# Performance work log

Measured on AMD Instinct MI355X. Metric: run time of the kernel, lower is better.

The kernel has to match this reference:

```python
import jax, jax.numpy as jnp
import numpy as np

B, S, E = 8, 4096, 512
QKV, H = 512, 8
D = QKV // H  # head_dim = 64
EPS = 1e-6


def setup_inputs() -> dict:
    key = jax.random.key(0)
    ks = jax.random.split(key, 9)
    sc_in = 1.0 / np.sqrt(E)
    sc_qkv = 1.0 / np.sqrt(QKV)
    # Linear weights stored as [in, out] so y = x @ W + b (equivalent to torch x @ W_t.T + b)
    return {
        "x": jax.random.normal(ks[0], (B, S, E), dtype=jnp.float32),
        "Wq": jax.random.uniform(ks[1], (E, QKV), jnp.float32, -sc_in, sc_in),
        "bq": jax.random.uniform(ks[2], (QKV,), jnp.float32, -sc_in, sc_in),
        "Wk": jax.random.uniform(ks[3], (E, QKV), jnp.float32, -sc_in, sc_in),
        "bk": jax.random.uniform(ks[4], (QKV,), jnp.float32, -sc_in, sc_in),
        "Wv": jax.random.uniform(ks[5], (E, QKV), jnp.float32, -sc_in, sc_in),
        "bv": jax.random.uniform(ks[6], (QKV,), jnp.float32, -sc_in, sc_in),
        "Wo": jax.random.uniform(ks[7], (QKV, E), jnp.float32, -sc_qkv, sc_qkv),
        "bo": jax.random.uniform(ks[8], (E,), jnp.float32, -sc_qkv, sc_qkv),
    }


def feature_map(t):
    # elu(x) + 1 (always positive features)
    return jax.nn.elu(t) + 1.0


def reference(x, Wq, bq, Wk, bk, Wv, bv, Wo, bo):
    bs, seqlen, _ = x.shape
    q = (x @ Wq + bq).reshape(bs, seqlen, H, D)
    k = (x @ Wk + bk).reshape(bs, seqlen, H, D)
    v = (x @ Wv + bv).reshape(bs, seqlen, H, D)
    q = feature_map(q)
    k = feature_map(k)
    # kv: [n, h, m, d] -- per-head outer-product accumulation over sequence
    kv = jnp.einsum('nshd,nshm->nhmd', k, v)
    # normalizer z: [n, l, h]
    z = 1.0 / (jnp.einsum('nlhd,nhd->nlh', q, k.sum(axis=1)) + EPS)
    out = jnp.einsum('nlhd,nhmd,nlh->nlhm', q, kv, z)
    out = out.reshape(bs, seqlen, QKV)
    return out @ Wo + bo
```

## Files before the change

kernel.cpp:

```cpp
#include <hip/hip_runtime.h>
#include <hip/hip_bf16.h>


typedef __bf16 bf16x8 __attribute__((ext_vector_type(8)));
typedef float  f32x4  __attribute__((ext_vector_type(4)));

__device__ __forceinline__ float b2f(unsigned short u) {
    unsigned int x = ((unsigned int)u) << 16;
    return __builtin_bit_cast(float, x);
}
__device__ __forceinline__ unsigned short f2b(float f) {
    unsigned int u = __builtin_bit_cast(unsigned int, f);
    unsigned int r = (u + 0x7FFFu + ((u >> 16) & 1u)) >> 16;
    return (unsigned short)r;
}
__device__ __forceinline__ void load_lds16(const unsigned short* g, unsigned short* l) {
    __builtin_amdgcn_global_load_lds(
        (const __attribute__((address_space(1))) void*)g,
        (__attribute__((address_space(3))) void*)l, 16, 0, 0);
}

__global__ void prep_kernel(const float* __restrict__ x,
                            const float* __restrict__ w0, const float* __restrict__ w1,
                            const float* __restrict__ w2, const float* __restrict__ w3,
                            unsigned short* __restrict__ xb, unsigned short* __restrict__ wt,
                            float* __restrict__ ksg, float* __restrict__ kvg) {
    __shared__ float tile[64][65];
    int t = threadIdx.x;
    if (blockIdx.x >= 256) {
        int i = (blockIdx.x - 256) * 256 + t;
        float4 v = ((const float4*)x)[i];
        ushort4 o;
        o.x = f2b(v.x); o.y = f2b(v.y); o.z = f2b(v.z); o.w = f2b(v.w);
        ((ushort4*)xb)[i] = o;
        return;
    }
    int idx = blockIdx.x;
    if (idx < 16) ksg[idx * 256 + t] = 0.f;
    ((float4*)kvg)[idx * 256 + t] = (float4){0.f, 0.f, 0.f, 0.f};
    int bz = idx >> 6, by = (idx >> 3) & 7, bx = idx & 7;
    const float* src = (bz == 0) ? w0 : (bz == 1) ? w1 : (bz == 2) ? w2 : w3;
    unsigned short* dst = wt + (size_t)bz * 512 * 512;
    int rb = by * 64, cb = bx * 64;
    #pragma unroll
    for (int i = 0; i < 16; i++) {
        int c = t + i * 256; int r = c >> 6, cc = c & 63;
        tile[r][cc] = src[(rb + r) * 512 + cb + cc];
    }
    __syncthreads();
    #pragma unroll
    for (int i = 0; i < 16; i++) {
        int c = t + i * 256; int r = c >> 6, cc = c & 63;
        dst[(cb + r) * 512 + rb + cc] = f2b(tile[cc][r]);
    }
}

__global__ __launch_bounds__(256, 4) void gemm_qkv_kernel(
        const unsigned short* __restrict__ xb, const unsigned short* __restrict__ wt,
        const float* __restrict__ bq, const float* __restrict__ bk, const float* __restrict__ bv,
        unsigned short* __restrict__ qb, unsigned short* __restrict__ kT,
        unsigned short* __restrict__ vT, float* __restrict__ ksg) {
    int g = blockIdx.x;
    int xcd = g & 7, slot = g >> 3;
    int mtile = xcd * 32 + slot / 12;
    int tn = slot % 12;
    int tensor = tn >> 2, ntile = tn & 3;
    const unsigned short* Bt = wt + (size_t)tensor * 512 * 512;
    const float* bias = tensor == 0 ? bq : tensor == 1 ? bk : bv;
    bool act = tensor < 2;

    __shared__ __align__(16) unsigned short sA[128 * 64];
    __shared__ __align__(16) unsigned short sB[128 * 64];
    const int tid  = threadIdx.x;
    const int wave = tid >> 6, lane = tid & 63;
    const int wm = wave >> 1, wn = wave & 1;
    const int quad = lane >> 4, l16 = lane & 15;
    const int mbase = mtile * 128, nbase = ntile * 128;
    const int rsub = lane >> 3;
    const int coff = (((lane & 7) ^ rsub) << 3);

    f32x4 acc[4][4];
    #pragma unroll
    for (int i = 0; i < 4; i++)
        #pragma unroll
        for (int j = 0; j < 4; j++) acc[i][j] = (f32x4){0.f, 0.f, 0.f, 0.f};

    for (int kb = 0; kb < 512; kb += 64) {
        #pragma unroll
        for (int t = 0; t < 4; t++) {
            int r0 = t * 32 + wave * 8;
            load_lds16(&xb[(size_t)(mbase + r0 + rsub) * 512 + kb + coff], &sA[r0 * 64]);
            load_lds16(&Bt[(size_t)(nbase + r0 + rsub) * 512 + kb + coff], &sB[r0 * 64]);
        }
        __syncthreads();
        #pragma unroll
        for (int ko = 0; ko < 64; ko += 32) {
            bf16x8 af[4], bfr[4];
            int pg = ((quad + (ko >> 3)) ^ (l16 & 7)) << 3;
            #pragma unroll
            for (int f = 0; f < 4; f++)
                af[f] = *(const bf16x8*)&sA[(wm * 64 + f * 16 + l16) * 64 + pg];
            #pragma unroll
            for (int f = 0; f < 4; f++)
                bfr[f] = *(const bf16x8*)&sB[(wn * 64 + f * 16 + l16) * 64 + pg];
            #pragma unroll
            for (int i = 0; i < 4; i++)
                #pragma unroll
                for (int j = 0; j < 4; j++)
                    acc[i][j] = __builtin_amdgcn_mfma_f32_16x16x32_bf16(af[i], bfr[j], acc[i][j], 0, 0, 0);
        }
        __syncthreads();
    }
    if (tensor == 0) {
        #pragma unroll
        for (int i = 0; i < 4; i++)
            #pragma unroll
            for (int j = 0; j < 4; j++) {
                int gcol = nbase + wn * 64 + j * 16 + l16;
                float bv = bias[gcol];
                #pragma unroll
                for (int r = 0; r < 4; r++) {
                    int grow = mbase + wm * 64 + i * 16 + quad * 4 + r;
                    float v = acc[i][j][r] + bv;
                    v = v > 0.f ? v + 1.f : __expf(v);
                    qb[(size_t)grow * 512 + gcol] = f2b(v);
                }
            }
    } else {
        unsigned short* T = (tensor == 1) ? kT : vT;
        float csum[4] = {0.f, 0.f, 0.f, 0.f};
        #pragma unroll
        for (int i = 0; i < 4; i++)
            #pragma unroll
            for (int j = 0; j < 4; j++) {
                int gcol = nbase + wn * 64 + j * 16 + l16;
                int h = gcol >> 6, d = gcol & 63;
                float bv = bias[gcol];
                int grow0 = mbase + wm * 64 + i * 16 + quad * 4;
                int b = grow0 >> 12, s0 = grow0 & 4095;
                ushort4 o;
                #pragma unroll
                for (int r = 0; r < 4; r++) {
                    float v = acc[i][j][r] + bv;
                    if (act) { v = v > 0.f ? v + 1.f : __expf(v); csum[j] += v; }
                    ((unsigned short*)&o)[r] = f2b(v);
                }
                *(ushort4*)&T[(((size_t)b * 8 + h) * 64 + d) * 4096 + s0] = o;
            }
        if (act) {
            int b = mbase >> 12;
            #pragma unroll
            for (int j = 0; j < 4; j++) {
                float s = csum[j];
                s += __shfl_xor(s, 16, 64);
                s += __shfl_xor(s, 32, 64);
                if (quad == 0) {
                    int gcol = nbase + wn * 64 + j * 16 + l16;
                    atomicAdd(&ksg[b * 512 + gcol], s);
                }
            }
        }
    }
}

__global__ __launch_bounds__(256, 2) void kv_kernel(
        const unsigned short* __restrict__ kT, const unsigned short* __restrict__ vT,
        float* __restrict__ kvg) {
    int bh = blockIdx.x >> 3, sc = blockIdx.x & 7;
    const int tid = threadIdx.x;
    const int wave = tid >> 6, lane = tid & 63;
    const int wm = wave >> 1, wn = wave & 1;
    const int quad = lane >> 4, l16 = lane & 15;
    const int rsub = lane >> 3;
    const int coff = (((lane & 7) ^ rsub) << 3);
    __shared__ __align__(16) unsigned short sV[2][64 * 64];
    __shared__ __align__(16) unsigned short sK[2][64 * 64];

    f32x4 acc[2][2];
    #pragma unroll
    for (int i = 0; i < 2; i++)
        #pragma unroll
        for (int j = 0; j < 2; j++) acc[i][j] = (f32x4){0.f, 0.f, 0.f, 0.f};
    size_t base = (size_t)bh * 64 * 4096 + sc * 512;

    auto stage = [&](int kb, int buf) {
        int s0 = kb * 64;
        #pragma unroll
        for (int t = 0; t < 2; t++) {
            int r0 = t * 32 + wave * 8;
            load_lds16(&vT[base + (size_t)(r0 + rsub) * 4096 + s0 + coff], &sV[buf][r0 * 64]);
            load_lds16(&kT[base + (size_t)(r0 + rsub) * 4096 + s0 + coff], &sK[buf][r0 * 64]);
        }
    };

    stage(0, 0);
    for (int kb = 0; kb < 8; kb++) {
        int buf = kb & 1;
        if (kb < 7) {
            stage(kb + 1, buf ^ 1);
            asm volatile("s_waitcnt vmcnt(4)" ::: "memory");
        } else {
            asm volatile("s_waitcnt vmcnt(0)" ::: "memory");
        }
        __builtin_amdgcn_sched_barrier(0);
        __builtin_amdgcn_s_barrier();
        #pragma unroll
        for (int ko = 0; ko < 64; ko += 32) {
            bf16x8 af[2], bfr[2];
            int pg = ((quad + (ko >> 3)) ^ (l16 & 7)) << 3;
            #pragma unroll
            for (int f = 0; f < 2; f++)
                af[f] = *(const bf16x8*)&sV[buf][(wm * 32 + f * 16 + l16) * 64 + pg];
            #pragma unroll
            for (int f = 0; f < 2; f++)
                bfr[f] = *(const bf16x8*)&sK[buf][(wn * 32 + f * 16 + l16) * 64 + pg];
            #pragma unroll
            for (int i = 0; i < 2; i++)
                #pragma unroll
                for (int j = 0; j < 2; j++)
                    acc[i][j] = __builtin_amdgcn_mfma_f32_16x16x32_bf16(af[i], bfr[j], acc[i][j], 0, 0, 0);
        }
        __builtin_amdgcn_s_barrier();
        __builtin_amdgcn_sched_barrier(0);
    }
    float* out = kvg + (size_t)bh * 4096;
    #pragma unroll
    for (int i = 0; i < 2; i++)
        #pragma unroll
        for (int j = 0; j < 2; j++)
            #pragma unroll
            for (int r = 0; r < 4; r++) {
                int m = wm * 32 + i * 16 + quad * 4 + r;
                int d = wn * 32 + j * 16 + l16;
                atomicAdd(&out[m * 64 + d], acc[i][j][r]);
            }
}

__global__ __launch_bounds__(256, 2) void fused_out_kernel(
        const unsigned short* __restrict__ qb,
        const float* __restrict__ kvg, const float* __restrict__ ksg,
        const unsigned short* __restrict__ wto, const float* __restrict__ bo,
        float* __restrict__ out) {
    int g = blockIdx.x;
    int xcd = g & 7, slot = g >> 3;
    int mtile = xcd * 32 + (slot >> 1);
    int np = slot & 1;

    __shared__ __align__(16) unsigned short sQ[128 * 64];
    __shared__ __align__(16) unsigned short sWo[2][128 * 64];
    __shared__ __align__(16) unsigned short sKV[64 * 64];
    __shared__ __align__(16) unsigned short sO1[128 * 64];
    __shared__ float sKsum[512];
    __shared__ float sZ[128];
    const int tid  = threadIdx.x;
    const int wave = tid >> 6, lane = tid & 63;
    const int wm = wave >> 1, wn = wave & 1;
    const int quad = lane >> 4, l16 = lane & 15;
    const int mbase = mtile * 128, nbase = np * 256;
    const int b = mtile >> 5;
    const int rsub = lane >> 3;
    const int coff = (((lane & 7) ^ rsub) << 3);

    sKsum[tid]       = ksg[b * 512 + tid];
    sKsum[tid + 256] = ksg[b * 512 + 256 + tid];

    f32x4 accm[2][4][4];
    #pragma unroll
    for (int n = 0; n < 2; n++)
        #pragma unroll
        for (int i = 0; i < 4; i++)
            #pragma unroll
            for (int j = 0; j < 4; j++) accm[n][i][j] = (f32x4){0.f, 0.f, 0.f, 0.f};

    for (int h = 0; h < 8; h++) {
        #pragma unroll
        for (int t = 0; t < 4; t++) {
            int r0 = t * 32 + wave * 8;
            load_lds16(&qb[(size_t)(mbase + r0 + rsub) * 512 + h * 64 + coff], &sQ[r0 * 64]);
            load_lds16(&wto[(size_t)(nbase + r0 + rsub) * 512 + h * 64 + coff], &sWo[0][r0 * 64]);
            load_lds16(&wto[(size_t)(nbase + 128 + r0 + rsub) * 512 + h * 64 + coff], &sWo[1][r0 * 64]);
        }
        #pragma unroll
        for (int oi = 0; oi < 2; oi++) {
            int idx = tid + oi * 256;
            int row = idx >> 3, G = idx & 7;
            const float4* src = (const float4*)&kvg[((size_t)(b * 8 + h)) * 4096 + row * 64 + G * 8];
            float4 a = src[0], c = src[1];
            unsigned int p0 = (unsigned int)f2b(a.x) | ((unsigned int)f2b(a.y) << 16);
            unsigned int p1 = (unsigned int)f2b(a.z) | ((unsigned int)f2b(a.w) << 16);
            unsigned int p2 = (unsigned int)f2b(c.x) | ((unsigned int)f2b(c.y) << 16);
            unsigned int p3 = (unsigned int)f2b(c.z) | ((unsigned int)f2b(c.w) << 16);
            *(uint4*)&sKV[row * 64 + ((G ^ (row & 7)) << 3)] = (uint4){p0, p1, p2, p3};
        }
        __syncthreads();
        {
            int row = tid >> 1, half = tid & 1;
            const float* ksh = &sKsum[h * 64];
            float dsum = 0.f;
            #pragma unroll
            for (int g2 = 0; g2 < 4; g2++) {
                int G = half * 4 + g2;
                uint4 w = *(const uint4*)&sQ[row * 64 + ((G ^ (row & 7)) << 3)];
                const unsigned int* qp = (const unsigned int*)&w;
                #pragma unroll
                for (int u = 0; u < 4; u++) {
                    int c = G * 8 + u * 2;
                    dsum += __builtin_bit_cast(float, qp[u] << 16)        * ksh[c];
                    dsum += __builtin_bit_cast(float, qp[u] & 0xFFFF0000u) * ksh[c + 1];
                }
            }
            dsum += __shfl_xor(dsum, 1, 64);
            if (!half) sZ[row] = 1.f / (dsum + 1e-6f);
        }
        __syncthreads();
        f32x4 acco[4][2];
        #pragma unroll
        for (int f = 0; f < 4; f++)
            #pragma unroll
            for (int j = 0; j < 2; j++) acco[f][j] = (f32x4){0.f, 0.f, 0.f, 0.f};
        #pragma unroll
        for (int ko = 0; ko < 64; ko += 32) {
            bf16x8 af[4], bfr[2];
            int pg = ((quad + (ko >> 3)) ^ (l16 & 7)) << 3;
            #pragma unroll
            for (int f = 0; f < 4; f++)
                af[f] = *(const bf16x8*)&sQ[(wm * 64 + f * 16 + l16) * 64 + pg];
            #pragma unroll
            for (int j = 0; j < 2; j++)
                bfr[j] = *(const bf16x8*)&sKV[(wn * 32 + j * 16 + l16) * 64 + pg];
            #pragma unroll
            for (int f = 0; f < 4; f++)
                #pragma unroll
                for (int j = 0; j < 2; j++)
                    acco[f][j] = __builtin_amdgcn_mfma_f32_16x16x32_bf16(af[f], bfr[j], acco[f][j], 0, 0, 0);
        }
        #pragma unroll
        for (int f = 0; f < 4; f++)
            #pragma unroll
            for (int j = 0; j < 2; j++)
                #pragma unroll
                for (int r = 0; r < 4; r++) {
                    int row = wm * 64 + f * 16 + quad * 4 + r;
                    int col = wn * 32 + j * 16 + l16;
                    float v = acco[f][j][r] * sZ[row];
                    int grp = col >> 3;
                    sO1[row * 64 + ((grp ^ (row & 7)) << 3) + (col & 7)] = f2b(v);
                }
        __syncthreads();
        #pragma unroll
        for (int ko = 0; ko < 64; ko += 32) {
            bf16x8 af[4], bfr0[4], bfr1[4];
            int pg = ((quad + (ko >> 3)) ^ (l16 & 7)) << 3;
            #pragma unroll
            for (int f = 0; f < 4; f++)
                af[f] = *(const bf16x8*)&sO1[(wm * 64 + f * 16 + l16) * 64 + pg];
            #pragma unroll
            for (int f = 0; f < 4; f++) {
                bfr0[f] = *(const bf16x8*)&sWo[0][(wn * 64 + f * 16 + l16) * 64 + pg];
                bfr1[f] = *(const bf16x8*)&sWo[1][(wn * 64 + f * 16 + l16) * 64 + pg];
            }
            #pragma unroll
            for (int i = 0; i < 4; i++)
                #pragma unroll
                for (int j = 0; j < 4; j++) {
                    accm[0][i][j] = __builtin_amdgcn_mfma_f32_16x16x32_bf16(af[i], bfr0[j], accm[0][i][j], 0, 0, 0);
                    accm[1][i][j] = __builtin_amdgcn_mfma_f32_16x16x32_bf16(af[i], bfr1[j], accm[1][i][j], 0, 0, 0);
                }
        }
        __syncthreads();
    }
    #pragma unroll
    for (int n = 0; n < 2; n++)
        #pragma unroll
        for (int i = 0; i < 4; i++)
            #pragma unroll
            for (int j = 0; j < 4; j++) {
                int gcol = nbase + n * 128 + wn * 64 + j * 16 + l16;
                float bv = bo[gcol];
                #pragma unroll
                for (int r = 0; r < 4; r++) {
                    int grow = mbase + wm * 64 + i * 16 + quad * 4 + r;
                    out[(size_t)grow * 512 + gcol] = accm[n][i][j][r] + bv;
                }
            }
}

extern "C" void kernel_launch(void* const* d_in, const int* in_sizes, int n_in,
                              void* d_out, int out_size, void* d_ws, size_t ws_size,
                              hipStream_t stream) {
    const float* x  = (const float*)d_in[0];
    const float* Wq = (const float*)d_in[1];
    const float* bq = (const float*)d_in[2];
    const float* Wk = (const float*)d_in[3];
    const float* bk = (const float*)d_in[4];
    const float* Wv = (const float*)d_in[5];
    const float* bv = (const float*)d_in[6];
    const float* Wo = (const float*)d_in[7];
    const float* bo = (const float*)d_in[8];
    float* out = (float*)d_out;

    char* wsb = (char*)d_ws;
    char* ob  = (char*)d_out;
    unsigned short* vT  = (unsigned short*)ob;
    unsigned short* xb  = (unsigned short*)(ob + 33554432ull);
    unsigned short* qb  = (unsigned short*)wsb;
    unsigned short* kT  = (unsigned short*)(wsb + 33554432ull);
    unsigned short* wt  = (unsigned short*)(wsb + 67108864ull);
    float*          kvg = (float*)(wsb + 69206016ull);
    float*          ksg = (float*)(wsb + 70254592ull);

    prep_kernel<<<16640, 256, 0, stream>>>(x, Wq, Wk, Wv, Wo, xb, wt, ksg, kvg);
    gemm_qkv_kernel<<<3072, 256, 0, stream>>>(xb, wt, bq, bk, bv, qb, kT, vT, ksg);
    kv_kernel<<<512, 256, 0, stream>>>(kT, vT, kvg);
    fused_out_kernel<<<512, 256, 0, stream>>>(qb, kvg, ksg,
            wt + 3ull * 512 * 512, bo, out);
}
```

Baseline: 249.2 us.

## Fuse K/V projection with per-tile KV outer-product accumulation in LDS

Splits the QKV projection into a Q-only GEMM and a K/V kernel that computes K and V tiles in sequence for the same row tile. The K/V tiles are kept in swizzled LDS, and their per-head outer product is accumulated into kv with atomics. This removes the global write and re-read of the transposed K and V tensors and drops the separate kv kernel. In exchange it adds many more float atomics into kv (one set per 128-row tile) and uses more LDS, which lowers occupancy to 2 blocks per CU.

Result: no change. 252.7 us (+1.4%).

```diff
diff --git a/kernel.cpp b/kernel.cpp
--- a/kernel.cpp
+++ b/kernel.cpp
@@ -5,10 +5,6 @@
 typedef __bf16 bf16x8 __attribute__((ext_vector_type(8)));
 typedef float  f32x4  __attribute__((ext_vector_type(4)));
 
-__device__ __forceinline__ float b2f(unsigned short u) {
-    unsigned int x = ((unsigned int)u) << 16;
-    return __builtin_bit_cast(float, x);
-}
 __device__ __forceinline__ unsigned short f2b(float f) {
     unsigned int u = __builtin_bit_cast(unsigned int, f);
     unsigned int r = (u + 0x7FFFu + ((u >> 16) & 1u)) >> 16;
@@ -55,19 +51,159 @@
     }
 }
 
-__global__ __launch_bounds__(256, 4) void gemm_qkv_kernel(
+__global__ __launch_bounds__(256, 2) void gemm_kv_kernel(
         const unsigned short* __restrict__ xb, const unsigned short* __restrict__ wt,
-        const float* __restrict__ bq, const float* __restrict__ bk, const float* __restrict__ bv,
-        unsigned short* __restrict__ qb, unsigned short* __restrict__ kT,
-        unsigned short* __restrict__ vT, float* __restrict__ ksg) {
+        const float* __restrict__ bk, const float* __restrict__ bv,
+        float* __restrict__ ksg, float* __restrict__ kvg) {
     int g = blockIdx.x;
     int xcd = g & 7, slot = g >> 3;
-    int mtile = xcd * 32 + slot / 12;
-    int tn = slot % 12;
-    int tensor = tn >> 2, ntile = tn & 3;
-    const unsigned short* Bt = wt + (size_t)tensor * 512 * 512;
-    const float* bias = tensor == 0 ? bq : tensor == 1 ? bk : bv;
-    bool act = tensor < 2;
+    int mtile = xcd * 32 + (slot >> 2);
+    int ntile = slot & 3;
+
+    __shared__ __align__(16) unsigned short sStage[16384];
+    __shared__ __align__(16) unsigned short sKT[16384];
+    unsigned short* sA = sStage;
+    unsigned short* sB = sStage + 8192;
+
+    const int tid  = threadIdx.x;
+    const int wave = tid >> 6, lane = tid & 63;
+    const int wm = wave >> 1, wn = wave & 1;
+    const int quad = lane >> 4, l16 = lane & 15;
+    const int mbase = mtile * 128, nbase = ntile * 128;
+    const int rsub = lane >> 3;
+    const int coff = (((lane & 7) ^ rsub) << 3);
+    const int b = mtile >> 5;
+
+    f32x4 acc[4][4];
+
+    auto run_pass = [&](const unsigned short* Bt) {
+        #pragma unroll
+        for (int i = 0; i < 4; i++)
+            #pragma unroll
+            for (int j = 0; j < 4; j++) acc[i][j] = (f32x4){0.f, 0.f, 0.f, 0.f};
+        for (int kb = 0; kb < 512; kb += 64) {
+            #pragma unroll
+            for (int t = 0; t < 4; t++) {
+                int r0 = t * 32 + wave * 8;
+                load_lds16(&xb[(size_t)(mbase + r0 + rsub) * 512 + kb + coff], &sA[r0 * 64]);
+                load_lds16(&Bt[(size_t)(nbase + r0 + rsub) * 512 + kb + coff], &sB[r0 * 64]);
+            }
+            __syncthreads();
+            #pragma unroll
+            for (int ko = 0; ko < 64; ko += 32) {
+                bf16x8 af[4], bfr[4];
+                int pg = ((quad + (ko >> 3)) ^ (l16 & 7)) << 3;
+                #pragma unroll
+                for (int f = 0; f < 4; f++)
+                    af[f] = *(const bf16x8*)&sA[(wm * 64 + f * 16 + l16) * 64 + pg];
+                #pragma unroll
+                for (int f = 0; f < 4; f++)
+                    bfr[f] = *(const bf16x8*)&sB[(wn * 64 + f * 16 + l16) * 64 + pg];
+                #pragma unroll
+                for (int i = 0; i < 4; i++)
+                    #pragma unroll
+                    for (int j = 0; j < 4; j++)
+                        acc[i][j] = __builtin_amdgcn_mfma_f32_16x16x32_bf16(af[i], bfr[j], acc[i][j], 0, 0, 0);
+            }
+            __syncthreads();
+        }
+    };
+
+    run_pass(wt + (size_t)1 * 512 * 512);
+    {
+        float csum[4] = {0.f, 0.f, 0.f, 0.f};
+        #pragma unroll
+        for (int i = 0; i < 4; i++)
+            #pragma unroll
+            for (int j = 0; j < 4; j++) {
+                int cb = wn * 64 + j * 16 + l16;
+                float bvv = bk[nbase + cb];
+                int s0 = wm * 64 + i * 16 + quad * 4;
+                ushort4 o;
+                #pragma unroll
+                for (int r = 0; r < 4; r++) {
+                    float v = acc[i][j][r] + bvv;
+                    v = v > 0.f ? v + 1.f : __expf(v);
+                    csum[j] += v;
+                    ((unsigned short*)&o)[r] = f2b(v);
+                }
+                *(ushort4*)&sKT[cb * 128 + (((s0 >> 3) ^ (cb & 7)) << 3) + (s0 & 7)] = o;
+            }
+        #pragma unroll
+        for (int j = 0; j < 4; j++) {
+            float s = csum[j];
+            s += __shfl_xor(s, 16, 64);
+            s += __shfl_xor(s, 32, 64);
+            if (quad == 0)
+                atomicAdd(&ksg[b * 512 + nbase + wn * 64 + j * 16 + l16], s);
+        }
+    }
+    run_pass(wt + (size_t)2 * 512 * 512);
+    {
+        #pragma unroll
+        for (int i = 0; i < 4; i++)
+            #pragma unroll
+            for (int j = 0; j < 4; j++) {
+                int cb = wn * 64 + j * 16 + l16;
+                float bvv = bv[nbase + cb];
+                int s0 = wm * 64 + i * 16 + quad * 4;
+                ushort4 o;
+                #pragma unroll
+                for (int r = 0; r < 4; r++)
+                    ((unsigned short*)&o)[r] = f2b(acc[i][j][r] + bvv);
+                *(ushort4*)&sStage[cb * 128 + (((s0 >> 3) ^ (cb & 7)) << 3) + (s0 & 7)] = o;
+            }
+    }
+    __syncthreads();
+    {
+        int hh = wave >> 1, rh = wave & 1;
+        f32x4 acc2[2][4];
+        #pragma unroll
+        for (int i = 0; i < 2; i++)
+            #pragma unroll
+            for (int j = 0; j < 4; j++) acc2[i][j] = (f32x4){0.f, 0.f, 0.f, 0.f};
+        #pragma unroll
+        for (int ko = 0; ko < 128; ko += 32) {
+            bf16x8 af[2], bfk[4];
+            int oct = (ko >> 3) + quad;
+            #pragma unroll
+            for (int i = 0; i < 2; i++) {
+                int row = hh * 64 + rh * 32 + i * 16 + l16;
+                af[i] = *(const bf16x8*)&sStage[row * 128 + ((oct ^ (row & 7)) << 3)];
+            }
+            #pragma unroll
+            for (int j = 0; j < 4; j++) {
+                int row = hh * 64 + j * 16 + l16;
+                bfk[j] = *(const bf16x8*)&sKT[row * 128 + ((oct ^ (row & 7)) << 3)];
+            }
+            #pragma unroll
+            for (int i = 0; i < 2; i++)
+                #pragma unroll
+                for (int j = 0; j < 4; j++)
+                    acc2[i][j] = __builtin_amdgcn_mfma_f32_16x16x32_bf16(af[i], bfk[j], acc2[i][j], 0, 0, 0);
+        }
+        int hg = ntile * 2 + hh;
+        float* dst = &kvg[((size_t)(b * 8 + hg)) * 4096];
+        #pragma unroll
+        for (int i = 0; i < 2; i++)
+            #pragma unroll
+            for (int j = 0; j < 4; j++)
+                #pragma unroll
+                for (int r = 0; r < 4; r++) {
+                    int m = rh * 32 + i * 16 + quad * 4 + r;
+                    int d = j * 16 + l16;
+                    atomicAdd(&dst[m * 64 + d], acc2[i][j][r]);
+                }
+    }
+}
+
+__global__ __launch_bounds__(256, 4) void gemm_q_kernel(
+        const unsigned short* __restrict__ xb, const unsigned short* __restrict__ wt,
+        const float* __restrict__ bq, unsigned short* __restrict__ qb) {
+    int g = blockIdx.x;
+    int xcd = g & 7, slot = g >> 3;
+    int mtile = xcd * 32 + (slot >> 2);
+    int ntile = slot & 3;
 
     __shared__ __align__(16) unsigned short sA[128 * 64];
     __shared__ __align__(16) unsigned short sB[128 * 64];
@@ -90,7 +226,7 @@
         for (int t = 0; t < 4; t++) {
             int r0 = t * 32 + wave * 8;
             load_lds16(&xb[(size_t)(mbase + r0 + rsub) * 512 + kb + coff], &sA[r0 * 64]);
-            load_lds16(&Bt[(size_t)(nbase + r0 + rsub) * 512 + kb + coff], &sB[r0 * 64]);
+            load_lds16(&wt[(size_t)(nbase + r0 + rsub) * 512 + kb + coff], &sB[r0 * 64]);
         }
         __syncthreads();
         #pragma unroll
@@ -111,129 +247,20 @@
         }
         __syncthreads();
     }
-    if (tensor == 0) {
-        #pragma unroll
-        for (int i = 0; i < 4; i++)
-            #pragma unroll
-            for (int j = 0; j < 4; j++) {
-                int gcol = nbase + wn * 64 + j * 16 + l16;
-                float bv = bias[gcol];
-                #pragma unroll
-                for (int r = 0; r < 4; r++) {
-                    int grow = mbase + wm * 64 + i * 16 + quad * 4 + r;
-                    float v = acc[i][j][r] + bv;
-                    v = v > 0.f ? v + 1.f : __expf(v);
-                    qb[(size_t)grow * 512 + gcol] = f2b(v);
-                }
-            }
-    } else {
-        unsigned short* T = (tensor == 1) ? kT : vT;
-        float csum[4] = {0.f, 0.f, 0.f, 0.f};
-        #pragma unroll
-        for (int i = 0; i < 4; i++)
-            #pragma unroll
-            for (int j = 0; j < 4; j++) {
-                int gcol = nbase + wn * 64 + j * 16 + l16;
-                int h = gcol >> 6, d = gcol & 63;
-                float bv = bias[gcol];
-                int grow0 = mbase + wm * 64 + i * 16 + quad * 4;
-                int b = grow0 >> 12, s0 = grow0 & 4095;
-                ushort4 o;
-                #pragma unroll
-                for (int r = 0; r < 4; r++) {
-                    float v = acc[i][j][r] + bv;
-                    if (act) { v = v > 0.f ? v + 1.f : __expf(v); csum[j] += v; }
-                    ((unsigned short*)&o)[r] = f2b(v);
-                }
-                *(ushort4*)&T[(((size_t)b * 8 + h) * 64 + d) * 4096 + s0] = o;
-            }
-        if (act) {
-            int b = mbase >> 12;
-            #pragma unroll
-            for (int j = 0; j < 4; j++) {
-                float s = csum[j];
-                s += __shfl_xor(s, 16, 64);
-                s += __shfl_xor(s, 32, 64);
-                if (quad == 0) {
-                    int gcol = nbase + wn * 64 + j * 16 + l16;
-                    atomicAdd(&ksg[b * 512 + gcol], s);
-                }
-            }
-        }
-    }
-}
-
-__global__ __launch_bounds__(256, 2) void kv_kernel(
-        const unsigned short* __restrict__ kT, const unsigned short* __restrict__ vT,
-        float* __restrict__ kvg) {
-    int bh = blockIdx.x >> 3, sc = blockIdx.x & 7;
-    const int tid = threadIdx.x;
-    const int wave = tid >> 6, lane = tid & 63;
-    const int wm = wave >> 1, wn = wave & 1;
-    const int quad = lane >> 4, l16 = lane & 15;
-    const int rsub = lane >> 3;
-    const int coff = (((lane & 7) ^ rsub) << 3);
-    __shared__ __align__(16) unsigned short sV[2][64 * 64];
-    __shared__ __align__(16) unsigned short sK[2][64 * 64];
-
-    f32x4 acc[2][2];
-    #pragma unroll
-    for (int i = 0; i < 2; i++)
-        #pragma unroll
-        for (int j = 0; j < 2; j++) acc[i][j] = (f32x4){0.f, 0.f, 0.f, 0.f};
-    size_t base = (size_t)bh * 64 * 4096 + sc * 512;
-
-    auto stage = [&](int kb, int buf) {
-        int s0 = kb * 64;
-        #pragma unroll
-        for (int t = 0; t < 2; t++) {
-            int r0 = t * 32 + wave * 8;
-            load_lds16(&vT[base + (size_t)(r0 + rsub) * 4096 + s0 + coff], &sV[buf][r0 * 64]);
-            load_lds16(&kT[base + (size_t)(r0 + rsub) * 4096 + s0 + coff], &sK[buf][r0 * 64]);
-        }
-    };
-
-    stage(0, 0);
-    for (int kb = 0; kb < 8; kb++) {
-        int buf = kb & 1;
-        if (kb < 7) {
-            stage(kb + 1, buf ^ 1);
-            asm volatile("s_waitcnt vmcnt(4)" ::: "memory");
-        } else {
-            asm volatile("s_waitcnt vmcnt(0)" ::: "memory");
-        }
-        __builtin_amdgcn_sched_barrier(0);
-        __builtin_amdgcn_s_barrier();
-        #pragma unroll
-        for (int ko = 0; ko < 64; ko += 32) {
-            bf16x8 af[2], bfr[2];
-            int pg = ((quad + (ko >> 3)) ^ (l16 & 7)) << 3;
-            #pragma unroll
-            for (int f = 0; f < 2; f++)
-                af[f] = *(const bf16x8*)&sV[buf][(wm * 32 + f * 16 + l16) * 64 + pg];
-            #pragma unroll
-            for (int f = 0; f < 2; f++)
-                bfr[f] = *(const bf16x8*)&sK[buf][(wn * 32 + f * 16 + l16) * 64 + pg];
-            #pragma unroll
-            for (int i = 0; i < 2; i++)
-                #pragma unroll
-                for (int j = 0; j < 2; j++)
-                    acc[i][j] = __builtin_amdgcn_mfma_f32_16x16x32_bf16(af[i], bfr[j], acc[i][j], 0, 0, 0);
-        }
-        __builtin_amdgcn_s_barrier();
-        __builtin_amdgcn_sched_barrier(0);
-    }
-    float* out = kvg + (size_t)bh * 4096;
-    #pragma unroll
-    for (int i = 0; i < 2; i++)
-        #pragma unroll
-        for (int j = 0; j < 2; j++)
+    #pragma unroll
+    for (int i = 0; i < 4; i++)
+        #pragma unroll
+        for (int j = 0; j < 4; j++) {
+            int gcol = nbase + wn * 64 + j * 16 + l16;
+            float bvv = bq[gcol];
             #pragma unroll
             for (int r = 0; r < 4; r++) {
-                int m = wm * 32 + i * 16 + quad * 4 + r;
-                int d = wn * 32 + j * 16 + l16;
-                atomicAdd(&out[m * 64 + d], acc[i][j][r]);
-            }
+                int grow = mbase + wm * 64 + i * 16 + quad * 4 + r;
+                float v = acc[i][j][r] + bvv;
+                v = v > 0.f ? v + 1.f : __expf(v);
+                qb[(size_t)grow * 512 + gcol] = f2b(v);
+            }
+        }
 }
 
 __global__ __launch_bounds__(256, 2) void fused_out_kernel(
@@ -376,11 +403,11 @@
             #pragma unroll
             for (int j = 0; j < 4; j++) {
                 int gcol = nbase + n * 128 + wn * 64 + j * 16 + l16;
-                float bv = bo[gcol];
+                float bvv = bo[gcol];
                 #pragma unroll
                 for (int r = 0; r < 4; r++) {
                     int grow = mbase + wm * 64 + i * 16 + quad * 4 + r;
-                    out[(size_t)grow * 512 + gcol] = accm[n][i][j][r] + bv;
+                    out[(size_t)grow * 512 + gcol] = accm[n][i][j][r] + bvv;
                 }
             }
 }
@@ -401,17 +428,15 @@
 
     char* wsb = (char*)d_ws;
     char* ob  = (char*)d_out;
-    unsigned short* vT  = (unsigned short*)ob;
-    unsigned short* xb  = (unsigned short*)(ob + 33554432ull);
+    unsigned short* xb  = (unsigned short*)ob;
     unsigned short* qb  = (unsigned short*)wsb;
-    unsigned short* kT  = (unsigned short*)(wsb + 33554432ull);
-    unsigned short* wt  = (unsigned short*)(wsb + 67108864ull);
-    float*          kvg = (float*)(wsb + 69206016ull);
-    float*          ksg = (float*)(wsb + 70254592ull);
+    unsigned short* wt  = (unsigned short*)(wsb + 33554432ull);
+    float*          kvg = (float*)(wsb + 35651584ull);
+    float*          ksg = (float*)(wsb + 36700160ull);
 
     prep_kernel<<<16640, 256, 0, stream>>>(x, Wq, Wk, Wv, Wo, xb, wt, ksg, kvg);
-    gemm_qkv_kernel<<<3072, 256, 0, stream>>>(xb, wt, bq, bk, bv, qb, kT, vT, ksg);
-    kv_kernel<<<512, 256, 0, stream>>>(kT, vT, kvg);
+    gemm_kv_kernel<<<1024, 256, 0, stream>>>(xb, wt, bk, bv, ksg, kvg);
+    gemm_q_kernel<<<1024, 256, 0, stream>>>(xb, wt, bq, qb);
     fused_out_kernel<<<512, 256, 0, stream>>>(qb, kvg, ksg,
             wt + 3ull * 512 * 512, bo, out);
 }
```

## Read KV and Wo fragments directly from global and prefetch next Q tile

Applied to the files above, without the earlier changes.

Drops the LDS staging buffers for the per-head KV matrix and the Wo tile. MFMA B-operands are now loaded from global memory into registers, with KV converted from fp32 to bf16 on the fly. The Q tile for the next head is prefetched into LDS while the output-projection GEMM runs, and one barrier per head is removed. The freed LDS is used to raise launch bounds to four blocks per CU. This aims to cut LDS traffic and barrier stalls and to raise occupancy. The risks are register spills, since the 128-float accumulator no longer fits comfortably, and extra redundant global/L2 reads of KV and Wo across waves.

Result: slower. 545.0 us (+118.7%).

```diff
diff --git a/kernel.cpp b/kernel.cpp
--- a/kernel.cpp
+++ b/kernel.cpp
@@ -5,10 +5,6 @@
 typedef __bf16 bf16x8 __attribute__((ext_vector_type(8)));
 typedef float  f32x4  __attribute__((ext_vector_type(4)));
 
-__device__ __forceinline__ float b2f(unsigned short u) {
-    unsigned int x = ((unsigned int)u) << 16;
-    return __builtin_bit_cast(float, x);
-}
 __device__ __forceinline__ unsigned short f2b(float f) {
     unsigned int u = __builtin_bit_cast(unsigned int, f);
     unsigned int r = (u + 0x7FFFu + ((u >> 16) & 1u)) >> 16;
@@ -236,7 +232,7 @@
             }
 }
 
-__global__ __launch_bounds__(256, 2) void fused_out_kernel(
+__global__ __launch_bounds__(256, 4) void fused_out_kernel(
         const unsigned short* __restrict__ qb,
         const float* __restrict__ kvg, const float* __restrict__ ksg,
         const unsigned short* __restrict__ wto, const float* __restrict__ bo,
@@ -247,8 +243,6 @@
     int np = slot & 1;
 
     __shared__ __align__(16) unsigned short sQ[128 * 64];
-    __shared__ __align__(16) unsigned short sWo[2][128 * 64];
-    __shared__ __align__(16) unsigned short sKV[64 * 64];
     __shared__ __align__(16) unsigned short sO1[128 * 64];
     __shared__ float sKsum[512];
     __shared__ float sZ[128];
@@ -272,26 +266,13 @@
             #pragma unroll
             for (int j = 0; j < 4; j++) accm[n][i][j] = (f32x4){0.f, 0.f, 0.f, 0.f};
 
+    #pragma unroll
+    for (int t = 0; t < 4; t++) {
+        int r0 = t * 32 + wave * 8;
+        load_lds16(&qb[(size_t)(mbase + r0 + rsub) * 512 + coff], &sQ[r0 * 64]);
+    }
+
     for (int h = 0; h < 8; h++) {
-        #pragma unroll
-        for (int t = 0; t < 4; t++) {
-            int r0 = t * 32 + wave * 8;
-            load_lds16(&qb[(size_t)(mbase + r0 + rsub) * 512 + h * 64 + coff], &sQ[r0 * 64]);
-            load_lds16(&wto[(size_t)(nbase + r0 + rsub) * 512 + h * 64 + coff], &sWo[0][r0 * 64]);
-            load_lds16(&wto[(size_t)(nbase + 128 + r0 + rsub) * 512 + h * 64 + coff], &sWo[1][r0 * 64]);
-        }
-        #pragma unroll
-        for (int oi = 0; oi < 2; oi++) {
-            int idx = tid + oi * 256;
-            int row = idx >> 3, G = idx & 7;
-            const float4* src = (const float4*)&kvg[((size_t)(b * 8 + h)) * 4096 + row * 64 + G * 8];
-            float4 a = src[0], c = src[1];
-            unsigned int p0 = (unsigned int)f2b(a.x) | ((unsigned int)f2b(a.y) << 16);
-            unsigned int p1 = (unsigned int)f2b(a.z) | ((unsigned int)f2b(a.w) << 16);
-            unsigned int p2 = (unsigned int)f2b(c.x) | ((unsigned int)f2b(c.y) << 16);
-            unsigned int p3 = (unsigned int)f2b(c.z) | ((unsigned int)f2b(c.w) << 16);
-            *(uint4*)&sKV[row * 64 + ((G ^ (row & 7)) << 3)] = (uint4){p0, p1, p2, p3};
-        }
         __syncthreads();
         {
             int row = tid >> 1, half = tid & 1;
@@ -312,12 +293,12 @@
             dsum += __shfl_xor(dsum, 1, 64);
             if (!half) sZ[row] = 1.f / (dsum + 1e-6f);
         }
-        __syncthreads();
         f32x4 acco[4][2];
         #pragma unroll
         for (int f = 0; f < 4; f++)
             #pragma unroll
             for (int j = 0; j < 2; j++) acco[f][j] = (f32x4){0.f, 0.f, 0.f, 0.f};
+        const float* kvh = &kvg[((size_t)(b * 8 + h)) * 4096];
         #pragma unroll
         for (int ko = 0; ko < 64; ko += 32) {
             bf16x8 af[4], bfr[2];
@@ -326,14 +307,24 @@
             for (int f = 0; f < 4; f++)
                 af[f] = *(const bf16x8*)&sQ[(wm * 64 + f * 16 + l16) * 64 + pg];
             #pragma unroll
-            for (int j = 0; j < 2; j++)
-                bfr[j] = *(const bf16x8*)&sKV[(wn * 32 + j * 16 + l16) * 64 + pg];
+            for (int j = 0; j < 2; j++) {
+                const float* kp = kvh + (wn * 32 + j * 16 + l16) * 64 + ko + quad * 8;
+                float4 ka = *(const float4*)kp;
+                float4 kb = *(const float4*)(kp + 4);
+                uint4 pk;
+                pk.x = (unsigned int)f2b(ka.x) | ((unsigned int)f2b(ka.y) << 16);
+                pk.y = (unsigned int)f2b(ka.z) | ((unsigned int)f2b(ka.w) << 16);
+                pk.z = (unsigned int)f2b(kb.x) | ((unsigned int)f2b(kb.y) << 16);
+                pk.w = (unsigned int)f2b(kb.z) | ((unsigned int)f2b(kb.w) << 16);
+                bfr[j] = __builtin_bit_cast(bf16x8, pk);
+            }
             #pragma unroll
             for (int f = 0; f < 4; f++)
                 #pragma unroll
                 for (int j = 0; j < 2; j++)
                     acco[f][j] = __builtin_amdgcn_mfma_f32_16x16x32_bf16(af[f], bfr[j], acco[f][j], 0, 0, 0);
         }
+        __syncthreads();
         #pragma unroll
         for (int f = 0; f < 4; f++)
             #pragma unroll
@@ -347,6 +338,13 @@
                     sO1[row * 64 + ((grp ^ (row & 7)) << 3) + (col & 7)] = f2b(v);
                 }
         __syncthreads();
+        if (h < 7) {
+            #pragma unroll
+            for (int t = 0; t < 4; t++) {
+                int r0 = t * 32 + wave * 8;
+                load_lds16(&qb[(size_t)(mbase + r0 + rsub) * 512 + (h + 1) * 64 + coff], &sQ[r0 * 64]);
+            }
+        }
         #pragma unroll
         for (int ko = 0; ko < 64; ko += 32) {
             bf16x8 af[4], bfr0[4], bfr1[4];
@@ -356,8 +354,8 @@
                 af[f] = *(const bf16x8*)&sO1[(wm * 64 + f * 16 + l16) * 64 + pg];
             #pragma unroll
             for (int f = 0; f < 4; f++) {
-                bfr0[f] = *(const bf16x8*)&sWo[0][(wn * 64 + f * 16 + l16) * 64 + pg];
-                bfr1[f] = *(const bf16x8*)&sWo[1][(wn * 64 + f * 16 + l16) * 64 + pg];
+                bfr0[f] = *(const bf16x8*)&wto[(size_t)(nbase + wn * 64 + f * 16 + l16) * 512 + h * 64 + ko + quad * 8];
+                bfr1[f] = *(const bf16x8*)&wto[(size_t)(nbase + 128 + wn * 64 + f * 16 + l16) * 512 + h * 64 + ko + quad * 8];
             }
             #pragma unroll
             for (int i = 0; i < 4; i++)
@@ -367,7 +365,6 @@
                     accm[1][i][j] = __builtin_amdgcn_mfma_f32_16x16x32_bf16(af[i], bfr1[j], accm[1][i][j], 0, 0, 0);
                 }
         }
-        __syncthreads();
     }
     #pragma unroll
     for (int n = 0; n < 2; n++)
@@ -376,11 +373,11 @@
             #pragma unroll
             for (int j = 0; j < 4; j++) {
                 int gcol = nbase + n * 128 + wn * 64 + j * 16 + l16;
-                float bv = bo[gcol];
+                float bvv = bo[gcol];
                 #pragma unroll
                 for (int r = 0; r < 4; r++) {
                     int grow = mbase + wm * 64 + i * 16 + quad * 4 + r;
-                    out[(size_t)grow * 512 + gcol] = accm[n][i][j][r] + bv;
+                    out[(size_t)grow * 512 + gcol] = accm[n][i][j][r] + bvv;
                 }
             }
 }
```
